# Performance work log

Hardware: AMD Instinct MI355X
Metric: run time of the kernel (lower is better)

## Reference

```python
import jax, jax.numpy as jnp
import numpy as np

B, S, D_IN, H, D_OUT = 32, 2048, 256, 512, 256


def setup_inputs() -> dict:
    key = jax.random.key(0)
    ks = jax.random.split(key, 12)
    sc = 0.02
    return {
        "x": jax.random.normal(ks[0], (B, S, D_IN), dtype=jnp.float32),
        # layer 0 (input_dim -> 4H), weights stored (in, out) so y = x @ W + b
        "Wx0": jax.random.normal(ks[1], (D_IN, 4 * H), dtype=jnp.float32) * sc,
        "bx0": jnp.zeros((4 * H,), dtype=jnp.float32),
        "Wh0": jax.random.normal(ks[2], (H, 4 * H), dtype=jnp.float32) * sc,
        "bh0": jnp.zeros((4 * H,), dtype=jnp.float32),
        # layer 1 (hidden -> 4H)
        "Wx1": jax.random.normal(ks[3], (H, 4 * H), dtype=jnp.float32) * sc,
        "bx1": jnp.zeros((4 * H,), dtype=jnp.float32),
        "Wh1": jax.random.normal(ks[4], (H, 4 * H), dtype=jnp.float32) * sc,
        "bh1": jnp.zeros((4 * H,), dtype=jnp.float32),
        # output projection
        "Wfc": jax.random.normal(ks[5], (H, D_OUT), dtype=jnp.float32) * sc,
        "bfc": jnp.zeros((D_OUT,), dtype=jnp.float32),
    }


def _cell(inp, h, c, Wx, bx, Wh, bh):
    # gates chunked in order f, i, g, o (matches torch chunk(4, dim=1))
    gates = inp @ Wx + bx + h @ Wh + bh  # [B, 4H]
    f, i, g, o = jnp.split(gates, 4, axis=1)
    c_new = jax.nn.sigmoid(f) * c + jax.nn.sigmoid(i) * jnp.tanh(g)
    h_new = jax.nn.sigmoid(o) * jnp.tanh(c_new)
    return h_new, c_new


def reference(x, Wx0, bx0, Wh0, bh0, Wx1, bx1, Wh1, bh1, Wfc, bfc):
    b = x.shape[0]
    hdim = Wh0.shape[0]

    def step(carry, xt):
        h0, c0, h1, c1 = carry
        h0, c0 = _cell(xt, h0, c0, Wx0, bx0, Wh0, bh0)
        h1, c1 = _cell(h0, h1, c1, Wx1, bx1, Wh1, bh1)
        return (h0, c0, h1, c1), h1

    init = tuple(jnp.zeros((b, hdim), x.dtype) for _ in range(4))
    x_tfirst = jnp.swapaxes(x, 0, 1)  # [S, B, D_in]
    _, outs = jax.lax.scan(step, init, x_tfirst)  # [S, B, H]
    outs = jnp.swapaxes(outs, 0, 1)  # [B, S, H]
    return outs @ Wfc + bfc  # [B, S, D_out]
```

## Files before the change

### kernel.cpp

```cpp
#include <hip/hip_runtime.h>
#include <math.h>

#define B_    32
#define S_    2048
#define DIN   256
#define H_    512
#define G_    2048
#define DOUT  256
#define T_    2048
#define NBLK  136

typedef __attribute__((ext_vector_type(8))) _Float16 f16x8;
typedef __attribute__((ext_vector_type(16))) float f32x16;

#define MFMA(a,b,c) __builtin_amdgcn_mfma_f32_32x32x16_f16((a),(b),(c),0,0,0)

#define OB_SLOT      0u
#define OB_H0H       16384u
#define OB_H1H       147456u
#define OB_STATE_END 278528u
#define OB_B0        278528u
#define OB_B1        286720u
#define OB_WF        294912u
#define OB_W0        557056u
#define OB_W1        3702784u
#define OB_END       7897088u
#define OB_XH        7897088u
#define OB_XEND      41451520u

#define LS_PT    65536
#define LS_CST   81920
#define LS_TOTAL 82944

__device__ __forceinline__ float sigf(float v) {
    return 1.0f / (1.0f + exp2f(-1.44269504f * v));
}
__device__ __forceinline__ float tanhfast(float v) {
    const float e = exp2f(2.88539008f * v);
    return 1.0f - 2.0f / (e + 1.0f);
}
__device__ __forceinline__ unsigned short h2u(_Float16 h) {
    union { _Float16 h; unsigned short u; } v; v.h = h; return v.u;
}

__device__ __forceinline__ f16x8 ld128_coh(const unsigned short* p) {
    f16x8 r;
    asm volatile("global_load_dwordx4 %0, %1, off sc0 sc1"
                 : "=v"(r) : "v"(p) : "memory");
    return r;
}
__device__ __forceinline__ int ld_slot(const int* slots, int i) {
    return __hip_atomic_load(&slots[i * 16], __ATOMIC_RELAXED, __HIP_MEMORY_SCOPE_AGENT);
}
__device__ __forceinline__ int packcol(int p) {
    return (((p >> 2) & 3) * H_) + ((p >> 4) << 2) + (p & 3);
}

__global__ __launch_bounds__(256) void repack_w(
    const float* __restrict__ s1, const float* __restrict__ s2,
    int k1, int K, int srcld, int dopack, unsigned short* __restrict__ dst)
{
    const int p  = blockIdx.x;
    const int kk = blockIdx.y * 256 + threadIdx.x;
    if (kk >= K) return;
    const int oc = dopack ? packcol(p) : p;
    const float w = (kk < k1) ? s1[(size_t)kk * srcld + oc]
                              : s2[(size_t)(kk - k1) * srcld + oc];
    dst[(size_t)p * K + kk] = h2u((_Float16)w);
}

__global__ __launch_bounds__(256) void repack_bias(
    const float* __restrict__ bx0, const float* __restrict__ bh0,
    const float* __restrict__ bx1, const float* __restrict__ bh1,
    char* __restrict__ wsb)
{
    const int q = blockIdx.x * 256 + threadIdx.x;
    if (q >= 2 * G_) return;
    const int p  = q & (G_ - 1);
    const int oc = packcol(p);
    float* dst = (float*)(wsb + (q < G_ ? OB_B0 : OB_B1));
    dst[p] = (q < G_) ? (bx0[oc] + bh0[oc]) : (bx1[oc] + bh1[oc]);
}

__global__ __launch_bounds__(256) void repack_x(const float* __restrict__ x, char* __restrict__ wsb)
{
    unsigned short* xh = (unsigned short*)(wsb + OB_XH);
    const size_t n = (size_t)B_ * S_ * DIN;
    for (size_t i = (size_t)blockIdx.x * 256 + threadIdx.x; i < n; i += (size_t)gridDim.x * 256)
        xh[i] = h2u((_Float16)x[i]);
}

template<int ROLE, int NSTEP>
__device__ __forceinline__ void phase_mm(
    int k0, int colc, int halfl, int t, int xsplit,
    const float* __restrict__ x, const unsigned short* __restrict__ XH,
    const unsigned short* A0, const unsigned short* A1,
    const unsigned short* Wlds, f32x16& acc)
{
    f16x8 fh[NSTEP];
    #pragma unroll
    for (int s = 0; s < NSTEP; ++s) {
        const int kf = k0 + s * 16;
        if (ROLE == 0 && kf < 256) {
            const size_t o = ((size_t)colc * S_ + t) * DIN + kf + halfl * 8;
            if (xsplit) {
                fh[s] = *(const f16x8*)(XH + o);
            } else {
                const float* xp = x + o;
                #pragma unroll
                for (int j = 0; j < 8; ++j) fh[s][j] = (_Float16)xp[j];
            }
        } else {
            const unsigned short* src; int kk;
            if (ROLE == 0)      { src = A1; kk = kf - 256; }
            else if (ROLE == 1) {
                if (kf < 512)   { src = A0; kk = kf; }
                else            { src = A1; kk = kf - 512; }
            } else              { src = A0; kk = kf; }
            fh[s] = ld128_coh(src + colc * 512 + kk + halfl * 8);
        }
    }
    asm volatile("s_waitcnt vmcnt(0)" ::: "memory");
    __builtin_amdgcn_sched_barrier(0);

    #pragma unroll
    for (int s = 0; s < NSTEP; ++s) {
        const int k8a = ((k0 + s * 16) >> 3) + halfl;
        const f16x8 bw = *(const f16x8*)(Wlds + (k8a * 32 + colc) * 8);
        acc = MFMA(fh[s], bw, acc);
    }
}

__global__ __launch_bounds__(512, 2) void lstm_persist(
    const float* __restrict__ x, const float* __restrict__ bfc,
    float* __restrict__ out, char* __restrict__ wsb, int xsplit)
{
    extern __shared__ char smem[];
    unsigned short* Wlds = (unsigned short*)smem;
    float* Pt   = (float*)(smem + LS_PT);
    float* cstL = (float*)(smem + LS_CST);
    int* slots  = (int*)(wsb + OB_SLOT);

    const int blk = blockIdx.x, tid = threadIdx.x;
    const int wave = tid >> 6, lane = tid & 63;
    const int colc = lane & 31, halfl = lane >> 5;

    int role, bb;
    if (blk < 64)       { role = 0; bb = blk; }
    else if (blk < 128) { role = 1; bb = blk - 64; }
    else                { role = 2; bb = blk - 128; }

    const int K  = (role == 0) ? 768 : (role == 1 ? 1024 : 512);
    const int p0 = bb * 32;

    {
        const unsigned short* Wg = (const unsigned short*)
            (wsb + (role == 0 ? OB_W0 : role == 1 ? OB_W1 : OB_WF));
        const int nk8 = K >> 3;
        for (int idx = tid; idx < nk8 * 32; idx += 512) {
            const int k8 = idx >> 5, cl = idx & 31;
            *(f16x8*)(Wlds + idx * 8) =
                *(const f16x8*)(Wg + ((size_t)(p0 + cl) * K + k8 * 8));
        }
    }
    for (int i = tid; i < 256; i += 512) cstL[i] = 0.f;
    __syncthreads();

    unsigned short* H0H = (unsigned short*)(wsb + OB_H0H);
    unsigned short* H1H = (unsigned short*)(wsb + OB_H1H);
    const unsigned short* XH = (const unsigned short*)(wsb + OB_XH);
    const float* Bp = (const float*)(wsb + (role == 1 ? OB_B1 : OB_B0));

    const int k0 = wave * (K >> 3);
    int sA = 0, sB = 0, sC = 0;

    for (int t = 0; t < T_; ++t) {
        if (tid < 64) {
            if (role == 0) {
                const int tA = t, tB = t - 3;
                for (;;) {
                    bool ok = true;
                    if (sA < tA) sA = ld_slot(slots, lane);
                    ok = ok && (sA >= tA);
                    if (sB < tB) sB = ld_slot(slots, 64 + lane);
                    ok = ok && (sB >= tB);
                    if (__all(ok)) break;
                    __builtin_amdgcn_s_sleep(1);
                }
            } else if (role == 1) {
                const int tA = t + 1, tB = t, tC = t - 3;
                for (;;) {
                    bool ok = true;
                    if (sA < tA) sA = ld_slot(slots, lane);
                    ok = ok && (sA >= tA);
                    if (sB < tB) sB = ld_slot(slots, 64 + lane);
                    ok = ok && (sB >= tB);
                    if (lane < 8) {
                        if (sC < tC) sC = ld_slot(slots, 128 + lane);
                        ok = ok && (sC >= tC);
                    }
                    if (__all(ok)) break;
                    __builtin_amdgcn_s_sleep(1);
                }
            } else {
                const int tA = t + 1;
                for (;;) {
                    if (sA < tA) sA = ld_slot(slots, 64 + lane);
                    if (__all(sA >= tA)) break;
                    __builtin_amdgcn_s_sleep(1);
                }
            }
        }
        __syncthreads();

        const int pw = t & 3, pr = (t + 3) & 3;
        const unsigned short *A0 = 0, *A1 = 0;
        if (role == 0)      { A1 = H0H + pr * 16384; }
        else if (role == 1) { A0 = H0H + pw * 16384; A1 = H1H + pr * 16384; }
        else                { A0 = H1H + pw * 16384; }

        f32x16 acc;
        #pragma unroll
        for (int i = 0; i < 16; ++i) acc[i] = 0.f;

        if (role == 0)
            phase_mm<0, 6>(k0, colc, halfl, t, xsplit, x, XH, A0, A1, Wlds, acc);
        else if (role == 1)
            phase_mm<1, 8>(k0, colc, halfl, t, xsplit, x, XH, A0, A1, Wlds, acc);
        else
            phase_mm<2, 4>(k0, colc, halfl, t, xsplit, x, XH, A0, A1, Wlds, acc);

        if (wave >= 4) {
            #pragma unroll
            for (int rg = 0; rg < 16; ++rg) {
                const int row = (rg & 3) + 8 * (rg >> 2) + 4 * halfl;
                Pt[(wave - 4) * 1024 + row * 32 + colc] = acc[rg];
            }
        }
        __syncthreads();
        if (wave < 4) {
            #pragma unroll
            for (int rg = 0; rg < 16; ++rg) {
                const int row = (rg & 3) + 8 * (rg >> 2) + 4 * halfl;
                Pt[wave * 1024 + row * 32 + colc] += acc[rg];
            }
        }
        __syncthreads();

        if (role == 2) {
            #pragma unroll
            for (int ii = 0; ii < 2; ++ii) {
                const int idx = tid * 2 + ii;
                const int r = idx >> 5, c = idx & 31;
                const float v = Pt[idx] + Pt[1024 + idx] + Pt[2048 + idx] + Pt[3072 + idx]
                              + bfc[p0 + c];
                out[((size_t)r * S_ + t) * DOUT + p0 + c] = v;
            }
        } else {
            #pragma unroll
            for (int ii = 0; ii < 2; ++ii) {
                const int idx = tid * 2 + ii;
                Pt[idx] = Pt[idx] + Pt[1024 + idx] + Pt[2048 + idx] + Pt[3072 + idx]
                        + Bp[p0 + (idx & 31)];
            }
            __syncthreads();
            if (tid < 128) {
                const int r = tid >> 2, u2 = (tid & 3) * 2;
                const int cb = ((u2 >> 2) << 4) + (u2 & 3);
                unsigned short uh[2];
                #pragma unroll
                for (int uu = 0; uu < 2; ++uu) {
                    const float fg = Pt[r * 32 + cb + uu + 0];
                    const float ig = Pt[r * 32 + cb + uu + 4];
                    const float gg = Pt[r * 32 + cb + uu + 8];
                    const float og = Pt[r * 32 + cb + uu + 12];
                    const float cv = cstL[r * 8 + u2 + uu];
                    const float cn = sigf(fg) * cv + sigf(ig) * tanhfast(gg);
                    const float hn = sigf(og) * tanhfast(cn);
                    cstL[r * 8 + u2 + uu] = cn;
                    uh[uu] = h2u((_Float16)hn);
                }
                const unsigned wv = (unsigned)uh[0] | ((unsigned)uh[1] << 16);
                const int off = pw * 16384 + r * 512 + bb * 8 + u2;
                unsigned short* DH = (role == 0) ? H0H : H1H;
                __hip_atomic_store((unsigned*)(DH + off), wv,
                                   __ATOMIC_RELAXED, __HIP_MEMORY_SCOPE_AGENT);
            }
        }

        __syncthreads();
        if (tid == 0)
            __hip_atomic_store(&slots[blk * 16], t + 1,
                               __ATOMIC_RELAXED, __HIP_MEMORY_SCOPE_AGENT);
    }
}

extern "C" void kernel_launch(void* const* d_in, const int* in_sizes, int n_in,
                              void* d_out, int out_size, void* d_ws, size_t ws_size,
                              hipStream_t stream)
{
    const float* x   = (const float*)d_in[0];
    const float* Wx0 = (const float*)d_in[1];
    const float* bx0 = (const float*)d_in[2];
    const float* Wh0 = (const float*)d_in[3];
    const float* bh0 = (const float*)d_in[4];
    const float* Wx1 = (const float*)d_in[5];
    const float* bx1 = (const float*)d_in[6];
    const float* Wh1 = (const float*)d_in[7];
    const float* bh1 = (const float*)d_in[8];
    const float* Wfc = (const float*)d_in[9];
    const float* bfc = (const float*)d_in[10];
    float* out = (float*)d_out;
    char*  wsb = (char*)d_ws;

    const int xsplit = (ws_size >= OB_XEND) ? 1 : 0;

    hipMemsetAsync(d_ws, 0, OB_STATE_END, stream);

    repack_w<<<dim3(G_, 3), 256, 0, stream>>>(Wx0, Wh0, 256, 768, G_, 1,
        (unsigned short*)(wsb + OB_W0));
    repack_w<<<dim3(G_, 4), 256, 0, stream>>>(Wx1, Wh1, 512, 1024, G_, 1,
        (unsigned short*)(wsb + OB_W1));
    repack_w<<<dim3(DOUT, 2), 256, 0, stream>>>(Wfc, Wfc, 512, 512, DOUT, 0,
        (unsigned short*)(wsb + OB_WF));
    repack_bias<<<16, 256, 0, stream>>>(bx0, bh0, bx1, bh1, wsb);
    if (xsplit) repack_x<<<2048, 256, 0, stream>>>(x, wsb);

    hipFuncSetAttribute((const void*)lstm_persist,
                        hipFuncAttributeMaxDynamicSharedMemorySize, LS_TOTAL);
    lstm_persist<<<NBLK, 512, LS_TOTAL, stream>>>(x, bfc, out, wsb, xsplit);
}
```

Before: 9.322 ms.

## Split layer-1 gate GEMM into separate input and recurrent partial blocks

Adds a new role of 64 blocks that computes the layer-1 input projection (h0 @ Wx1) and writes partial sums to a global buffer. The layer-1 recurrent blocks now compute only h1 @ Wh1 and add the stored partial. This halves the K of the layer-1 cell's critical-path matmul, so the input part can run ahead, off the h1 dependency chain. In exchange the grid grows from 136 to 200 blocks, and it adds an extra global round trip through coherent loads, extra slot synchronisation, and more co-resident blocks that could contend for CUs.

```diff
diff --git a/kernel.cpp b/kernel.cpp
--- a/kernel.cpp
+++ b/kernel.cpp
@@ -8,29 +8,31 @@
 #define G_    2048
 #define DOUT  256
 #define T_    2048
-#define NBLK  136
+#define NBLK  200
 
 typedef __attribute__((ext_vector_type(8))) _Float16 f16x8;
 typedef __attribute__((ext_vector_type(16))) float f32x16;
+typedef __attribute__((ext_vector_type(2))) float f32x2;
 
 #define MFMA(a,b,c) __builtin_amdgcn_mfma_f32_32x32x16_f16((a),(b),(c),0,0,0)
 
 #define OB_SLOT      0u
 #define OB_H0H       16384u
 #define OB_H1H       147456u
-#define OB_STATE_END 278528u
-#define OB_B0        278528u
-#define OB_B1        286720u
-#define OB_WF        294912u
-#define OB_W0        557056u
-#define OB_W1        3702784u
-#define OB_END       7897088u
-#define OB_XH        7897088u
-#define OB_XEND      41451520u
-
-#define LS_PT    65536
-#define LS_CST   81920
-#define LS_TOTAL 82944
+#define OB_PART      278528u
+#define OB_STATE_END 1327104u
+#define OB_B0        1327104u
+#define OB_B1        1335296u
+#define OB_WF        1343488u
+#define OB_W0        1605632u
+#define OB_W1        4751360u
+#define OB_END       8945664u
+#define OB_XH        8945664u
+#define OB_XEND      42500096u
+
+#define LS_PT    49152
+#define LS_CST   65536
+#define LS_TOTAL 66560
 
 __device__ __forceinline__ float sigf(float v) {
     return 1.0f / (1.0f + exp2f(-1.44269504f * v));
@@ -48,6 +50,16 @@
     asm volatile("global_load_dwordx4 %0, %1, off sc0 sc1"
                  : "=v"(r) : "v"(p) : "memory");
     return r;
+}
+__device__ __forceinline__ f32x2 ld64f_coh(const float* p) {
+    f32x2 r;
+    asm volatile("global_load_dwordx2 %0, %1, off sc0 sc1"
+                 : "=v"(r) : "v"(p) : "memory");
+    return r;
+}
+__device__ __forceinline__ void st64f_coh(float* p, f32x2 v) {
+    asm volatile("global_store_dwordx2 %0, %1, off sc0 sc1"
+                 :: "v"(p), "v"(v) : "memory");
 }
 __device__ __forceinline__ int ld_slot(const int* slots, int i) {
     return __hip_atomic_load(&slots[i * 16], __ATOMIC_RELAXED, __HIP_MEMORY_SCOPE_AGENT);
@@ -90,18 +102,16 @@
         xh[i] = h2u((_Float16)x[i]);
 }
 
-template<int ROLE, int NSTEP>
-__device__ __forceinline__ void phase_mm(
+__device__ __forceinline__ void phase_mm_l0(
     int k0, int colc, int halfl, int t, int xsplit,
     const float* __restrict__ x, const unsigned short* __restrict__ XH,
-    const unsigned short* A0, const unsigned short* A1,
-    const unsigned short* Wlds, f32x16& acc)
-{
-    f16x8 fh[NSTEP];
+    const unsigned short* A1, const unsigned short* Wlds, f32x16& acc)
+{
+    f16x8 fh[6];
     #pragma unroll
-    for (int s = 0; s < NSTEP; ++s) {
+    for (int s = 0; s < 6; ++s) {
         const int kf = k0 + s * 16;
-        if (ROLE == 0 && kf < 256) {
+        if (kf < 256) {
             const size_t o = ((size_t)colc * S_ + t) * DIN + kf + halfl * 8;
             if (xsplit) {
                 fh[s] = *(const f16x8*)(XH + o);
@@ -111,20 +121,31 @@
                 for (int j = 0; j < 8; ++j) fh[s][j] = (_Float16)xp[j];
             }
         } else {
-            const unsigned short* src; int kk;
-            if (ROLE == 0)      { src = A1; kk = kf - 256; }
-            else if (ROLE == 1) {
-                if (kf < 512)   { src = A0; kk = kf; }
-                else            { src = A1; kk = kf - 512; }
-            } else              { src = A0; kk = kf; }
-            fh[s] = ld128_coh(src + colc * 512 + kk + halfl * 8);
+            fh[s] = ld128_coh(A1 + colc * 512 + (kf - 256) + halfl * 8);
         }
     }
     asm volatile("s_waitcnt vmcnt(0)" ::: "memory");
     __builtin_amdgcn_sched_barrier(0);
-
     #pragma unroll
-    for (int s = 0; s < NSTEP; ++s) {
+    for (int s = 0; s < 6; ++s) {
+        const int k8a = ((k0 + s * 16) >> 3) + halfl;
+        const f16x8 bw = *(const f16x8*)(Wlds + (k8a * 32 + colc) * 8);
+        acc = MFMA(fh[s], bw, acc);
+    }
+}
+
+__device__ __forceinline__ void phase_mm_single(
+    int k0, int colc, int halfl,
+    const unsigned short* A, const unsigned short* Wlds, f32x16& acc)
+{
+    f16x8 fh[4];
+    #pragma unroll
+    for (int s = 0; s < 4; ++s)
+        fh[s] = ld128_coh(A + colc * 512 + (k0 + s * 16) + halfl * 8);
+    asm volatile("s_waitcnt vmcnt(0)" ::: "memory");
+    __builtin_amdgcn_sched_barrier(0);
+    #pragma unroll
+    for (int s = 0; s < 4; ++s) {
         const int k8a = ((k0 + s * 16) >> 3) + halfl;
         const f16x8 bw = *(const f16x8*)(Wlds + (k8a * 32 + colc) * 8);
         acc = MFMA(fh[s], bw, acc);
@@ -148,19 +169,22 @@
     int role, bb;
     if (blk < 64)       { role = 0; bb = blk; }
     else if (blk < 128) { role = 1; bb = blk - 64; }
-    else                { role = 2; bb = blk - 128; }
-
-    const int K  = (role == 0) ? 768 : (role == 1 ? 1024 : 512);
+    else if (blk < 192) { role = 2; bb = blk - 128; }
+    else                { role = 3; bb = blk - 192; }
+
     const int p0 = bb * 32;
 
     {
-        const unsigned short* Wg = (const unsigned short*)
-            (wsb + (role == 0 ? OB_W0 : role == 1 ? OB_W1 : OB_WF));
-        const int nk8 = K >> 3;
-        for (int idx = tid; idx < nk8 * 32; idx += 512) {
+        const unsigned short* Wg;
+        int wstride, rowoff, kcnt;
+        if (role == 0)      { Wg = (const unsigned short*)(wsb + OB_W0); wstride = 768;  rowoff = 0;   kcnt = 768; }
+        else if (role == 1) { Wg = (const unsigned short*)(wsb + OB_W1); wstride = 1024; rowoff = 0;   kcnt = 512; }
+        else if (role == 2) { Wg = (const unsigned short*)(wsb + OB_W1); wstride = 1024; rowoff = 512; kcnt = 512; }
+        else                { Wg = (const unsigned short*)(wsb + OB_WF); wstride = 512;  rowoff = 0;   kcnt = 512; }
+        for (int idx = tid; idx < (kcnt >> 3) * 32; idx += 512) {
             const int k8 = idx >> 5, cl = idx & 31;
             *(f16x8*)(Wlds + idx * 8) =
-                *(const f16x8*)(Wg + ((size_t)(p0 + cl) * K + k8 * 8));
+                *(const f16x8*)(Wg + ((size_t)(p0 + cl) * wstride + rowoff + k8 * 8));
         }
     }
     for (int i = tid; i < 256; i += 512) cstL[i] = 0.f;
@@ -168,10 +192,12 @@
 
     unsigned short* H0H = (unsigned short*)(wsb + OB_H0H);
     unsigned short* H1H = (unsigned short*)(wsb + OB_H1H);
+    float* PART = (float*)(wsb + OB_PART);
     const unsigned short* XH = (const unsigned short*)(wsb + OB_XH);
-    const float* Bp = (const float*)(wsb + (role == 1 ? OB_B1 : OB_B0));
-
-    const int k0 = wave * (K >> 3);
+    const float* Bp = (const float*)(wsb + (role == 2 ? OB_B1 : OB_B0));
+
+    const int kcnt = (role == 0) ? 768 : 512;
+    const int k0 = wave * (kcnt >> 3);
     int sA = 0, sB = 0, sC = 0;
 
     for (int t = 0; t < T_; ++t) {
@@ -188,15 +214,30 @@
                     __builtin_amdgcn_s_sleep(1);
                 }
             } else if (role == 1) {
-                const int tA = t + 1, tB = t, tC = t - 3;
+                const int tA = t + 1, tB = t - 3;
                 for (;;) {
                     bool ok = true;
                     if (sA < tA) sA = ld_slot(slots, lane);
                     ok = ok && (sA >= tA);
-                    if (sB < tB) sB = ld_slot(slots, 64 + lane);
-                    ok = ok && (sB >= tB);
+                    if (lane == 0) {
+                        if (sB < tB) sB = ld_slot(slots, 128 + bb);
+                        ok = ok && (sB >= tB);
+                    }
+                    if (__all(ok)) break;
+                    __builtin_amdgcn_s_sleep(1);
+                }
+            } else if (role == 2) {
+                const int tA = t, tB = t + 1, tC = t - 3;
+                for (;;) {
+                    bool ok = true;
+                    if (sA < tA) sA = ld_slot(slots, 128 + lane);
+                    ok = ok && (sA >= tA);
+                    if (lane == 0) {
+                        if (sB < tB) sB = ld_slot(slots, 64 + bb);
+                        ok = ok && (sB >= tB);
+                    }
                     if (lane < 8) {
-                        if (sC < tC) sC = ld_slot(slots, 128 + lane);
+                        if (sC < tC) sC = ld_slot(slots, 192 + lane);
                         ok = ok && (sC >= tC);
                     }
                     if (__all(ok)) break;
@@ -205,7 +246,7 @@
             } else {
                 const int tA = t + 1;
                 for (;;) {
-                    if (sA < tA) sA = ld_slot(slots, 64 + lane);
+                    if (sA < tA) sA = ld_slot(slots, 128 + lane);
                     if (__all(sA >= tA)) break;
                     __builtin_amdgcn_s_sleep(1);
                 }
@@ -214,21 +255,23 @@
         __syncthreads();
 
         const int pw = t & 3, pr = (t + 3) & 3;
-        const unsigned short *A0 = 0, *A1 = 0;
-        if (role == 0)      { A1 = H0H + pr * 16384; }
-        else if (role == 1) { A0 = H0H + pw * 16384; A1 = H1H + pr * 16384; }
-        else                { A0 = H1H + pw * 16384; }
+
+        f32x2 preg = {0.f, 0.f};
+        if (role == 2)
+            preg = ld64f_coh(PART + ((size_t)(pw * 64 + bb) << 10) + tid * 2);
 
         f32x16 acc;
         #pragma unroll
         for (int i = 0; i < 16; ++i) acc[i] = 0.f;
 
         if (role == 0)
-            phase_mm<0, 6>(k0, colc, halfl, t, xsplit, x, XH, A0, A1, Wlds, acc);
+            phase_mm_l0(k0, colc, halfl, t, xsplit, x, XH, H0H + pr * 16384, Wlds, acc);
         else if (role == 1)
-            phase_mm<1, 8>(k0, colc, halfl, t, xsplit, x, XH, A0, A1, Wlds, acc);
+            phase_mm_single(k0, colc, halfl, H0H + pw * 16384, Wlds, acc);
+        else if (role == 2)
+            phase_mm_single(k0, colc, halfl, H1H + pr * 16384, Wlds, acc);
         else
-            phase_mm<2, 4>(k0, colc, halfl, t, xsplit, x, XH, A0, A1, Wlds, acc);
+            phase_mm_single(k0, colc, halfl, H1H + pw * 16384, Wlds, acc);
 
         if (wave >= 4) {
             #pragma unroll
@@ -247,7 +290,15 @@
         }
         __syncthreads();
 
-        if (role == 2) {
+        if (role == 1) {
+            f32x2 pv;
+            #pragma unroll
+            for (int ii = 0; ii < 2; ++ii) {
+                const int idx = tid * 2 + ii;
+                pv[ii] = Pt[idx] + Pt[1024 + idx] + Pt[2048 + idx] + Pt[3072 + idx];
+            }
+            st64f_coh(PART + ((size_t)(pw * 64 + bb) << 10) + tid * 2, pv);
+        } else if (role == 3) {
             #pragma unroll
             for (int ii = 0; ii < 2; ++ii) {
                 const int idx = tid * 2 + ii;
@@ -260,8 +311,10 @@
             #pragma unroll
             for (int ii = 0; ii < 2; ++ii) {
                 const int idx = tid * 2 + ii;
-                Pt[idx] = Pt[idx] + Pt[1024 + idx] + Pt[2048 + idx] + Pt[3072 + idx]
+                float v = Pt[idx] + Pt[1024 + idx] + Pt[2048 + idx] + Pt[3072 + idx]
                         + Bp[p0 + (idx & 31)];
+                if (role == 2) v += preg[ii];
+                Pt[idx] = v;
             }
             __syncthreads();
             if (tid < 128) {
```

New measurement: 9.212 ms (median of 2 runs). About the same (-1.2%).
